# Performance work log

Hardware: AMD Instinct MI355X
Metric: run time of the kernel (lower is better)

## Reference

```python
import jax, jax.numpy as jnp
import numpy as np

N_NODES = 50000
N_EDGES = 800000
N_GRAPHS = 128
F_IN = 36
HEADS1 = 10
OUT_DIM = 128


def _gat_layer(x, src, dst, W, a_src, a_dst, b, heads, out_c):
    # x: [N, Fin]; W: [Fin, heads*out_c]; a_src/a_dst: [heads, out_c]; b: [heads*out_c]
    N = x.shape[0]
    h = (x @ W).reshape(N, heads, out_c)                      # [N,H,C]
    al_s = jnp.einsum('nhc,hc->nh', h, a_src)                 # [N,H]
    al_d = jnp.einsum('nhc,hc->nh', h, a_dst)                 # [N,H]
    e = jax.nn.leaky_relu(al_s[src] + al_d[dst], negative_slope=0.2)  # [E,H]
    # segment-softmax over incoming edges of each dst node
    m = jax.ops.segment_max(e, dst, num_segments=N)
    m = jnp.where(jnp.isfinite(m), m, 0.0)
    p = jnp.exp(e - m[dst])
    s = jax.ops.segment_sum(p, dst, num_segments=N)
    alpha = p / (s[dst] + 1e-16)                              # [E,H]
    out = jax.ops.segment_sum(alpha[:, :, None] * h[src], dst, num_segments=N)  # [N,H,C]
    return out.reshape(N, heads * out_c) + b


def setup_inputs() -> dict:
    key = jax.random.key(0)
    ks = jax.random.split(key, 12)
    x = jax.random.normal(ks[0], (N_NODES, F_IN), dtype=jnp.float32)
    edge_index = jax.random.randint(ks[1], (2, N_EDGES), 0, N_NODES, dtype=jnp.int64)
    batch = jnp.sort(jax.random.randint(ks[2], (N_NODES,), 0, N_GRAPHS, dtype=jnp.int64))
    g = 0.1  # glorot-ish scale
    W1 = jax.random.normal(ks[3], (F_IN, HEADS1 * F_IN), dtype=jnp.float32) * g
    att_src1 = jax.random.normal(ks[4], (HEADS1, F_IN), dtype=jnp.float32) * g
    att_dst1 = jax.random.normal(ks[5], (HEADS1, F_IN), dtype=jnp.float32) * g
    b1 = jnp.zeros((HEADS1 * F_IN,), dtype=jnp.float32)
    W2 = jax.random.normal(ks[6], (HEADS1 * F_IN, OUT_DIM), dtype=jnp.float32) * g
    att_src2 = jax.random.normal(ks[7], (1, OUT_DIM), dtype=jnp.float32) * g
    att_dst2 = jax.random.normal(ks[8], (1, OUT_DIM), dtype=jnp.float32) * g
    b2 = jnp.zeros((OUT_DIM,), dtype=jnp.float32)
    fc_w = jax.random.normal(ks[9], (OUT_DIM, OUT_DIM), dtype=jnp.float32) * g
    fc_b = jnp.zeros((OUT_DIM,), dtype=jnp.float32)
    return {"x": x, "edge_index": edge_index, "batch": batch,
            "W1": W1, "att_src1": att_src1, "att_dst1": att_dst1, "b1": b1,
            "W2": W2, "att_src2": att_src2, "att_dst2": att_dst2, "b2": b2,
            "fc_w": fc_w, "fc_b": fc_b}


def reference(x, edge_index, batch, W1, att_src1, att_dst1, b1,
              W2, att_src2, att_dst2, b2, fc_w, fc_b):
    N = x.shape[0]
    # PyG GATConv adds self loops by default
    loops = jnp.arange(N, dtype=edge_index.dtype)
    src = jnp.concatenate([edge_index[0], loops])
    dst = jnp.concatenate([edge_index[1], loops])
    # eval mode: dropouts are identity
    h = jax.nn.elu(_gat_layer(x, src, dst, W1, att_src1, att_dst1, b1, HEADS1, F_IN))
    h = _gat_layer(h, src, dst, W2, att_src2, att_dst2, b2, 1, OUT_DIM)
    h = jax.nn.relu(h)
    # global max pool over graphs
    g = jax.ops.segment_max(h, batch, num_segments=N_GRAPHS)
    g = jnp.where(jnp.isfinite(g), g, 0.0)
    out = jax.nn.relu(g @ fc_w + fc_b)
    return out
```

## Files before the change

kernel.cpp:

```cpp
#include <hip/hip_runtime.h>
#include <hip/hip_fp16.h>
#include <math.h>

#define N_NODES  50000
#define N_EDGES  800000
#define E_TOT    850000
#define N_GRAPHS 128
#define F_IN     36
#define NH1      10
#define C1       36
#define D1       360
#define D2       128

#define SCHUNK  512
#define NCHUNK  98

typedef unsigned int u32;

#if defined(__has_builtin)
#if __has_builtin(__builtin_amdgcn_fdot2)
#define HAVE_FDOT2 1
#endif
#endif
#ifndef HAVE_FDOT2
#define HAVE_FDOT2 0
#endif

typedef _Float16 h2v __attribute__((ext_vector_type(2)));

static __device__ __forceinline__ float2 h2f(u32 u) {
  __half2 h = __builtin_bit_cast(__half2, u);
  return __half22float2(h);
}
static __device__ __forceinline__ u32 f2h2(float a, float b) {
  __half2 h = __floats2half2_rn(a, b);
  return __builtin_bit_cast(u32, h);
}
static __device__ __forceinline__ float dot2acc(u32 a, u32 b, float acc) {
#if HAVE_FDOT2
  return __builtin_amdgcn_fdot2(__builtin_bit_cast(h2v, a), __builtin_bit_cast(h2v, b), acc, false);
#else
  float2 fa = h2f(a), fb = h2f(b);
  return fmaf(fa.x, fb.x, fmaf(fa.y, fb.y, acc));
#endif
}

__global__ void k_init(int* counts, u32* pool) {
  int i = blockIdx.x * blockDim.x + threadIdx.x;
  if (i < N_NODES) counts[i] = 0;
  if (i < N_GRAPHS * D2) pool[i] = 0u;
}

__global__ void k_hist(const int* ei, int* counts) {
  int e = blockIdx.x * blockDim.x + threadIdx.x;
  if (e >= E_TOT) return;
  int d = (e < N_EDGES) ? ei[N_EDGES + e] : (e - N_EDGES);
  atomicAdd(&counts[d], 1);
}

__global__ void k_scan1(const int* counts, int* partial) {
  __shared__ int red[256];
  int b = blockIdx.x, t = threadIdx.x;
  int base = b * SCHUNK;
  int v = 0;
  int i0 = base + t, i1 = base + t + 256;
  if (i0 < N_NODES) v += counts[i0];
  if (i1 < N_NODES) v += counts[i1];
  red[t] = v; __syncthreads();
  for (int off = 128; off; off >>= 1) {
    if (t < off) red[t] += red[t + off];
    __syncthreads();
  }
  if (t == 0) partial[b] = red[0];
}

__global__ void k_scan2(const int* partial, int* chunk_off, int* row_ptr) {
  if (threadIdx.x == 0 && blockIdx.x == 0) {
    int acc = 0;
    for (int i = 0; i < NCHUNK; i++) { chunk_off[i] = acc; acc += partial[i]; }
    row_ptr[N_NODES] = acc;
  }
}

__global__ void k_scan3(const int* counts, const int* chunk_off, int* row_ptr, int* nxt) {
  __shared__ int tmp[SCHUNK];
  int b = blockIdx.x, t = threadIdx.x;
  int i = b * SCHUNK + t;
  int v = (i < N_NODES) ? counts[i] : 0;
  tmp[t] = v; __syncthreads();
  for (int off = 1; off < SCHUNK; off <<= 1) {
    int x = (t >= off) ? tmp[t - off] : 0;
    __syncthreads();
    tmp[t] += x;
    __syncthreads();
  }
  if (i < N_NODES) {
    int excl = chunk_off[b] + tmp[t] - v;
    row_ptr[i] = excl;
    nxt[i] = excl;
  }
}

__global__ void k_scatter(const int* ei, int* nxt, int* csr_src) {
  int e = blockIdx.x * blockDim.x + threadIdx.x;
  if (e >= E_TOT) return;
  int s, d;
  if (e < N_EDGES) { s = ei[e]; d = ei[N_EDGES + e]; }
  else             { s = d = e - N_EDGES; }
  int pos = atomicAdd(&nxt[d], 1);
  csr_src[pos] = s;
}

__global__ void k_wals(const float* __restrict__ W1, const float* __restrict__ asrc,
                       const float* __restrict__ adst, float* w_als, float* w_ald) {
  int i = blockIdx.x * blockDim.x + threadIdx.x;
  if (i >= D1) return;
  int h = i / F_IN, k = i - h * F_IN;
  float sa = 0.f, sd = 0.f;
  for (int c = 0; c < C1; c++) {
    float wv = W1[k * D1 + h * C1 + c];
    sa = fmaf(wv, asrc[h * C1 + c], sa);
    sd = fmaf(wv, adst[h * C1 + c], sd);
  }
  w_als[i] = sa; w_ald[i] = sd;
}

__global__ void k_w1t2(const float* __restrict__ W1, u32* __restrict__ W1t2) {
  int i = blockIdx.x * blockDim.x + threadIdx.x;
  if (i >= D1 * (F_IN / 2)) return;
  int hc = i / (F_IN / 2), kp = i - hc * (F_IN / 2);
  W1t2[i] = f2h2(W1[(2 * kp) * D1 + hc], W1[(2 * kp + 1) * D1 + hc]);
}

__global__ void k_xh(const float* __restrict__ x, u32* __restrict__ xh2) {
  int i = blockIdx.x * blockDim.x + threadIdx.x;
  if (i >= N_NODES * F_IN / 2) return;
  xh2[i] = f2h2(x[2 * i], x[2 * i + 1]);
}

__global__ void k_packw2(const float* __restrict__ W2, u32* __restrict__ W2h) {
  int i = blockIdx.x * blockDim.x + threadIdx.x;
  if (i >= (D1 / 2) * D2) return;
  int kp = i / D2, col = i - kp * D2;
  W2h[i] = f2h2(W2[(2 * kp) * D2 + col], W2[(2 * kp + 1) * D2 + col]);
}

__global__ __launch_bounds__(256)
void k_als1(const float* __restrict__ x, const float* __restrict__ w_als,
            const float* __restrict__ w_ald, float* als, float* ald) {
  __shared__ float xs[64][F_IN + 1];
  __shared__ float wa[D1], wd[D1];
  int t = threadIdx.x;
  int nb = blockIdx.x * 64;
  for (int i = t; i < D1; i += 256) { wa[i] = w_als[i]; wd[i] = w_ald[i]; }
  int lim = min(64, N_NODES - nb);
  for (int i = t; i < lim * F_IN; i += 256) {
    int n = i / F_IN, k = i - n * F_IN;
    xs[n][k] = x[(size_t)(nb + n) * F_IN + k];
  }
  __syncthreads();
  for (int pair = t; pair < lim * NH1; pair += 256) {
    int n = pair / NH1, h = pair - n * NH1;
    const float* xp = xs[n];
    const float* wap = &wa[h * F_IN];
    const float* wdp = &wd[h * F_IN];
    float sa = 0.f, sd = 0.f;
#pragma unroll
    for (int k = 0; k < F_IN; k++) {
      float xv = xp[k];
      sa = fmaf(xv, wap[k], sa);
      sd = fmaf(xv, wdp[k], sd);
    }
    als[(size_t)(nb + n) * NH1 + h] = sa;
    ald[(size_t)(nb + n) * NH1 + h] = sd;
  }
}

__global__ __launch_bounds__(256)
void k_agg1(const __half* __restrict__ xh, const float* __restrict__ als,
            const float* __restrict__ ald, const int* __restrict__ row_ptr,
            const int* __restrict__ csr_src, __half* __restrict__ aggxh) {
  __shared__ float pl[4][64][NH1];
  __shared__ int ssrc[4][64];
  int w = threadIdx.x >> 6, lane = threadIdx.x & 63;
  int node = blockIdx.x * 4 + w;
  int beg = row_ptr[node], end = row_ptr[node + 1];

  int ch[6], hd[6];
#pragma unroll
  for (int j = 0; j < 6; j++) {
    int slot = lane + 64 * j;
    if (slot >= D1) slot = D1 - 1;
    hd[j] = slot / C1;
    ch[j] = slot - hd[j] * C1;
  }
  bool v5 = (lane < D1 - 320);

  float aldn[NH1];
#pragma unroll
  for (int h = 0; h < NH1; h++) aldn[h] = ald[(size_t)node * NH1 + h];
  float acc[6] = {0.f, 0.f, 0.f, 0.f, 0.f, 0.f};
  float sp[NH1];
#pragma unroll
  for (int h = 0; h < NH1; h++) sp[h] = 0.f;

  for (int base = beg; base < end; base += 64) {
    int cnt = min(64, end - base);
    float p[NH1];
    int msrc = 0;
    if (lane < cnt) {
      msrc = csr_src[base + lane];
      const float2* ap = (const float2*)(als + (size_t)msrc * NH1);
#pragma unroll
      for (int q = 0; q < 5; q++) {
        float2 v = ap[q];
        float v0 = v.x + aldn[2 * q];
        float v1 = v.y + aldn[2 * q + 1];
        v0 = v0 > 0.f ? v0 : 0.2f * v0;
        v1 = v1 > 0.f ? v1 : 0.2f * v1;
        p[2 * q] = __expf(v0);
        p[2 * q + 1] = __expf(v1);
      }
    } else {
#pragma unroll
      for (int h = 0; h < NH1; h++) p[h] = 0.f;
    }
#pragma unroll
    for (int h = 0; h < NH1; h++) sp[h] += p[h];
    ssrc[w][lane] = msrc;
    float2* plw = (float2*)pl[w][lane];
#pragma unroll
    for (int q = 0; q < 5; q++) plw[q] = float2{p[2 * q], p[2 * q + 1]};
    __builtin_amdgcn_wave_barrier();

    for (int j = 0; j < cnt; j++) {
      int srcj = ssrc[w][j];
      const __half* row = xh + (size_t)srcj * F_IN;
      const float* plj = pl[w][j];
#pragma unroll
      for (int jj = 0; jj < 6; jj++) {
        if (jj < 5 || v5) {
          float xv = __half2float(row[ch[jj]]);
          acc[jj] = fmaf(plj[hd[jj]], xv, acc[jj]);
        }
      }
    }
    __builtin_amdgcn_wave_barrier();
  }

#pragma unroll
  for (int h = 0; h < NH1; h++) {
    float t = sp[h];
#pragma unroll
    for (int off = 32; off; off >>= 1) t += __shfl_xor(t, off);
    sp[h] = t;
  }
#pragma unroll
  for (int jj = 0; jj < 6; jj++) {
    if (jj < 5 || v5) {
      float inv = 1.f / (sp[hd[jj]] + 1e-16f);
      aggxh[(size_t)node * D1 + lane + 64 * jj] = __float2half(acc[jj] * inv);
    }
  }
}

#define MIX_NPB 32
__global__ __launch_bounds__(384)
void k_mix1(const u32* __restrict__ aggx2, const u32* __restrict__ W1t2,
            const float* __restrict__ b1, __half* __restrict__ hact) {
  __shared__ u32 ag[MIX_NPB][D1 / 2 + 4];
  int t = threadIdx.x;
  int nb = blockIdx.x * MIX_NPB;
  int lim = min(MIX_NPB, N_NODES - nb);
  const u32* gsrc = aggx2 + (size_t)nb * (D1 / 2);
  for (int i = t; i < lim * (D1 / 2); i += 384) {
    int n = i / (D1 / 2), k = i - n * (D1 / 2);
    ag[n][k] = gsrc[i];
  }
  __syncthreads();
  if (t < D1) {
    int h = t / C1;
    u32 wreg[F_IN / 2];
#pragma unroll
    for (int kp = 0; kp < F_IN / 2; kp++) wreg[kp] = W1t2[t * (F_IN / 2) + kp];
    float bj = b1[t];
    for (int n = 0; n < lim; n++) {
      const u32* a = &ag[n][h * (F_IN / 2)];
      float acc2 = 0.f;
#pragma unroll
      for (int kp = 0; kp < F_IN / 2; kp++) acc2 = dot2acc(a[kp], wreg[kp], acc2);
      float val = acc2 + bj;
      val = val > 0.f ? val : __expf(val) - 1.f;
      hact[(size_t)(nb + n) * D1 + t] = __float2half(val);
    }
  }
}

#define G2_NPB 16
__global__ __launch_bounds__(256)
void k_gemm2(const __half* __restrict__ hacth, const u32* __restrict__ W2h,
             __half* __restrict__ h2h) {
  __shared__ u32 hs2[D1 / 2][G2_NPB];
  int nb = blockIdx.x * G2_NPB;
  int t = threadIdx.x;
  for (int i = t; i < G2_NPB * (D1 / 2); i += 256) {
    int n = i / (D1 / 2), kp = i - n * (D1 / 2);
    hs2[kp][n] = ((const u32*)(hacth + (size_t)(nb + n) * D1))[kp];
  }
  __syncthreads();
  int col = t & 127, ng = t >> 7;
  float acc[8];
#pragma unroll
  for (int i = 0; i < 8; i++) acc[i] = 0.f;
#pragma unroll 2
  for (int kp = 0; kp < D1 / 2; kp++) {
    u32 wv = W2h[kp * D2 + col];
    uint4 r0 = *(const uint4*)&hs2[kp][ng * 8];
    uint4 r1 = *(const uint4*)&hs2[kp][ng * 8 + 4];
    acc[0] = dot2acc(r0.x, wv, acc[0]);
    acc[1] = dot2acc(r0.y, wv, acc[1]);
    acc[2] = dot2acc(r0.z, wv, acc[2]);
    acc[3] = dot2acc(r0.w, wv, acc[3]);
    acc[4] = dot2acc(r1.x, wv, acc[4]);
    acc[5] = dot2acc(r1.y, wv, acc[5]);
    acc[6] = dot2acc(r1.z, wv, acc[6]);
    acc[7] = dot2acc(r1.w, wv, acc[7]);
  }
#pragma unroll
  for (int i = 0; i < 8; i++)
    h2h[(size_t)(nb + ng * 8 + i) * D2 + col] = __float2half(acc[i]);
}

__global__ void k_als2(const __half* __restrict__ h2h, const float* __restrict__ asrc,
                       const float* __restrict__ adst, float* als, float* ald) {
  int node = blockIdx.x * 4 + (threadIdx.x >> 6);
  int lane = threadIdx.x & 63;
  const u32* hr = (const u32*)(h2h + (size_t)node * D2);
  float2 f = h2f(hr[lane]);
  float2 a = ((const float2*)asrc)[lane];
  float2 d = ((const float2*)adst)[lane];
  float ps = f.x * a.x + f.y * a.y;
  float pd = f.x * d.x + f.y * d.y;
#pragma unroll
  for (int off = 32; off; off >>= 1) { ps += __shfl_xor(ps, off); pd += __shfl_xor(pd, off); }
  if (lane == 0) { als[node] = ps; ald[node] = pd; }
}

__global__ __launch_bounds__(256)
void k_agg2(const __half* __restrict__ h2h, const float* __restrict__ als,
            const float* __restrict__ ald, const int* __restrict__ row_ptr,
            const int* __restrict__ csr_src, const float* __restrict__ b2,
            const int* __restrict__ batch, u32* __restrict__ pool) {
  int w = threadIdx.x >> 6, lane = threadIdx.x & 63;
  int node = blockIdx.x * 4 + w;
  int beg = row_ptr[node], end = row_ptr[node + 1];
  float aldn = ald[node];
  float ax = 0.f, ay = 0.f, ssum = 0.f;
  for (int base = beg; base < end; base += 64) {
    int cnt = min(64, end - base);
    int msrc = 0; float p = 0.f;
    if (lane < cnt) {
      msrc = csr_src[base + lane];
      float vv = als[msrc] + aldn;
      vv = vv > 0.f ? vv : 0.2f * vv;
      p = __expf(vv);
    }
    ssum += p;
    int j2 = 0;
    for (; j2 + 2 <= cnt; j2 += 2) {
      int sA = __shfl(msrc, j2), sB = __shfl(msrc, j2 + 1);
      float cA = __shfl(p, j2), cB = __shfl(p, j2 + 1);
      u32 ua = ((const u32*)(h2h + (size_t)sA * D2))[lane];
      u32 ub = ((const u32*)(h2h + (size_t)sB * D2))[lane];
      float2 f = h2f(ua); ax = fmaf(cA, f.x, ax); ay = fmaf(cA, f.y, ay);
      f = h2f(ub); ax = fmaf(cB, f.x, ax); ay = fmaf(cB, f.y, ay);
    }
    if (j2 < cnt) {
      int sA = __shfl(msrc, j2);
      float cA = __shfl(p, j2);
      u32 ua = ((const u32*)(h2h + (size_t)sA * D2))[lane];
      float2 f = h2f(ua); ax = fmaf(cA, f.x, ax); ay = fmaf(cA, f.y, ay);
    }
  }
  float t2 = ssum;
#pragma unroll
  for (int off = 32; off; off >>= 1) t2 += __shfl_xor(t2, off);
  float inv = 1.f / (t2 + 1e-16f);
  float2 bv = ((const float2*)b2)[lane];
  float vx = fmaxf(ax * inv + bv.x, 0.f);
  float vy = fmaxf(ay * inv + bv.y, 0.f);
  int g = batch[node];
  atomicMax(&pool[g * D2 + 2 * lane], __float_as_uint(vx));
  atomicMax(&pool[g * D2 + 2 * lane + 1], __float_as_uint(vy));
}

__global__ void k_final(const float* __restrict__ pool, const float* __restrict__ fcw,
                        const float* __restrict__ fcb, float* __restrict__ out) {
  __shared__ float ps[D2];
  int g = blockIdx.x, j = threadIdx.x;
  ps[j] = pool[g * D2 + j];
  __syncthreads();
  float acc = 0.f;
  for (int c = 0; c < D2; c++) acc = fmaf(ps[c], fcw[c * D2 + j], acc);
  acc += fcb[j];
  out[g * D2 + j] = acc > 0.f ? acc : 0.f;
}

extern "C" void kernel_launch(void* const* d_in, const int* in_sizes, int n_in,
                              void* d_out, int out_size, void* d_ws, size_t ws_size,
                              hipStream_t stream) {
  const float* x     = (const float*)d_in[0];
  const int*   ei    = (const int*)d_in[1];
  const int*   batch = (const int*)d_in[2];
  const float* W1    = (const float*)d_in[3];
  const float* asrc1 = (const float*)d_in[4];
  const float* adst1 = (const float*)d_in[5];
  const float* b1    = (const float*)d_in[6];
  const float* W2    = (const float*)d_in[7];
  const float* asrc2 = (const float*)d_in[8];
  const float* adst2 = (const float*)d_in[9];
  const float* b2    = (const float*)d_in[10];
  const float* fcw   = (const float*)d_in[11];
  const float* fcb   = (const float*)d_in[12];
  float* out = (float*)d_out;

  char* w = (char*)d_ws;
  size_t off = 0;
  auto alloc = [&](size_t bytes) -> char* {
    char* p = w + off;
    off = (off + bytes + 255) & ~(size_t)255;
    return p;
  };
  int* counts    = (int*)alloc((size_t)N_NODES * 4);
  int* row_ptr   = (int*)alloc((size_t)(N_NODES + 1) * 4);
  int* nxt       = (int*)alloc((size_t)N_NODES * 4);
  int* csr_src   = (int*)alloc((size_t)E_TOT * 4);
  int* partial   = (int*)alloc(NCHUNK * 4);
  int* chunk_off = (int*)alloc(NCHUNK * 4);
  float* als1    = (float*)alloc((size_t)N_NODES * NH1 * 4);
  float* ald1    = (float*)alloc((size_t)N_NODES * NH1 * 4);
  float* als2    = (float*)alloc((size_t)N_NODES * 4);
  float* ald2    = (float*)alloc((size_t)N_NODES * 4);
  u32*   pool    = (u32*)alloc((size_t)N_GRAPHS * D2 * 4);
  float* w_als   = (float*)alloc((size_t)D1 * 4);
  float* w_ald   = (float*)alloc((size_t)D1 * 4);
  u32*   W1t2    = (u32*)alloc((size_t)D1 * (F_IN / 2) * 4);
  u32*   W2h     = (u32*)alloc((size_t)(D1 / 2) * D2 * 4);
  u32*   xh2     = (u32*)alloc((size_t)N_NODES * (F_IN / 2) * 4);
  u32*   aggx2   = (u32*)alloc((size_t)N_NODES * (D1 / 2) * 4);
  __half* hacth  = (__half*)alloc((size_t)N_NODES * D1 * 2);
  __half* h2h    = (__half*)alloc((size_t)N_NODES * D2 * 2);

  k_init<<<dim3(196), dim3(256), 0, stream>>>(counts, pool);
  k_hist<<<dim3((E_TOT + 255) / 256), dim3(256), 0, stream>>>(ei, counts);
  k_scan1<<<dim3(NCHUNK), dim3(256), 0, stream>>>(counts, partial);
  k_scan2<<<dim3(1), dim3(64), 0, stream>>>(partial, chunk_off, row_ptr);
  k_scan3<<<dim3(NCHUNK), dim3(SCHUNK), 0, stream>>>(counts, chunk_off, row_ptr, nxt);
  k_scatter<<<dim3((E_TOT + 255) / 256), dim3(256), 0, stream>>>(ei, nxt, csr_src);

  k_wals<<<dim3(2), dim3(256), 0, stream>>>(W1, asrc1, adst1, w_als, w_ald);
  k_w1t2<<<dim3((D1 * (F_IN / 2) + 255) / 256), dim3(256), 0, stream>>>(W1, W1t2);
  k_packw2<<<dim3(((D1 / 2) * D2 + 255) / 256), dim3(256), 0, stream>>>(W2, W2h);
  k_xh<<<dim3((N_NODES * F_IN / 2 + 255) / 256), dim3(256), 0, stream>>>(x, xh2);

  k_als1<<<dim3((N_NODES + 63) / 64), dim3(256), 0, stream>>>(x, w_als, w_ald, als1, ald1);
  k_agg1<<<dim3(N_NODES / 4), dim3(256), 0, stream>>>((const __half*)xh2, als1, ald1,
                                                      row_ptr, csr_src, (__half*)aggx2);
  k_mix1<<<dim3((N_NODES + MIX_NPB - 1) / MIX_NPB), dim3(384), 0, stream>>>(aggx2, W1t2, b1, hacth);

  k_gemm2<<<dim3(N_NODES / G2_NPB), dim3(256), 0, stream>>>(hacth, W2h, h2h);
  k_als2<<<dim3(N_NODES / 4), dim3(256), 0, stream>>>(h2h, asrc2, adst2, als2, ald2);
  k_agg2<<<dim3(N_NODES / 4), dim3(256), 0, stream>>>(h2h, als2, ald2, row_ptr, csr_src,
                                                      b2, batch, pool);

  k_final<<<dim3(N_GRAPHS), dim3(D2), 0, stream>>>((const float*)pool, fcw, fcb, out);

  (void)in_sizes; (void)n_in; (void)out_size; (void)ws_size;
}
```

Before: 552.0 us.

## Fuse weight prep kernels, fold x half-conversion into als1, vectorize agg1 gather

Merges the three weight-preparation kernels into one launch and moves the x-to-half conversion into k_als1, which already stages x in shared memory. This removes several launches and one extra pass over x. The layer-1 aggregation now has each lane handle half2 channel pairs (3 slots per lane instead of 6 scalar halves) and broadcasts source indices via shuffles instead of shared memory. It also unrolls the neighbor loop by two to raise memory-level parallelism, at the cost of more registers.

```diff
diff --git a/kernel.cpp b/kernel.cpp
--- a/kernel.cpp
+++ b/kernel.cpp
@@ -11,6 +11,7 @@
 #define C1       36
 #define D1       360
 #define D2       128
+#define XW       18
 
 #define SCHUNK  512
 #define NCHUNK  98
@@ -111,43 +112,34 @@
   csr_src[pos] = s;
 }
 
-__global__ void k_wals(const float* __restrict__ W1, const float* __restrict__ asrc,
-                       const float* __restrict__ adst, float* w_als, float* w_ald) {
-  int i = blockIdx.x * blockDim.x + threadIdx.x;
-  if (i >= D1) return;
-  int h = i / F_IN, k = i - h * F_IN;
-  float sa = 0.f, sd = 0.f;
-  for (int c = 0; c < C1; c++) {
-    float wv = W1[k * D1 + h * C1 + c];
-    sa = fmaf(wv, asrc[h * C1 + c], sa);
-    sd = fmaf(wv, adst[h * C1 + c], sd);
-  }
-  w_als[i] = sa; w_ald[i] = sd;
-}
-
-__global__ void k_w1t2(const float* __restrict__ W1, u32* __restrict__ W1t2) {
-  int i = blockIdx.x * blockDim.x + threadIdx.x;
-  if (i >= D1 * (F_IN / 2)) return;
-  int hc = i / (F_IN / 2), kp = i - hc * (F_IN / 2);
-  W1t2[i] = f2h2(W1[(2 * kp) * D1 + hc], W1[(2 * kp + 1) * D1 + hc]);
-}
-
-__global__ void k_xh(const float* __restrict__ x, u32* __restrict__ xh2) {
-  int i = blockIdx.x * blockDim.x + threadIdx.x;
-  if (i >= N_NODES * F_IN / 2) return;
-  xh2[i] = f2h2(x[2 * i], x[2 * i + 1]);
-}
-
-__global__ void k_packw2(const float* __restrict__ W2, u32* __restrict__ W2h) {
-  int i = blockIdx.x * blockDim.x + threadIdx.x;
-  if (i >= (D1 / 2) * D2) return;
-  int kp = i / D2, col = i - kp * D2;
-  W2h[i] = f2h2(W2[(2 * kp) * D2 + col], W2[(2 * kp + 1) * D2 + col]);
+__global__ void k_prep(const float* __restrict__ W1, const float* __restrict__ asrc,
+                       const float* __restrict__ adst, const float* __restrict__ W2,
+                       float* w_als, float* w_ald, u32* W1t2, u32* W2h) {
+  int id = blockIdx.x * blockDim.x + threadIdx.x;
+  if (id < D1) {
+    int h = id / F_IN, k = id - h * F_IN;
+    float sa = 0.f, sd = 0.f;
+    for (int c = 0; c < C1; c++) {
+      float wv = W1[k * D1 + h * C1 + c];
+      sa = fmaf(wv, asrc[h * C1 + c], sa);
+      sd = fmaf(wv, adst[h * C1 + c], sd);
+    }
+    w_als[id] = sa; w_ald[id] = sd;
+  } else if (id < D1 + D1 * (F_IN / 2)) {
+    int i = id - D1;
+    int hc = i / (F_IN / 2), kp = i - hc * (F_IN / 2);
+    W1t2[i] = f2h2(W1[(2 * kp) * D1 + hc], W1[(2 * kp + 1) * D1 + hc]);
+  } else if (id < D1 + D1 * (F_IN / 2) + (D1 / 2) * D2) {
+    int i = id - D1 - D1 * (F_IN / 2);
+    int kp = i / D2, col = i - kp * D2;
+    W2h[i] = f2h2(W2[(2 * kp) * D2 + col], W2[(2 * kp + 1) * D2 + col]);
+  }
 }
 
 __global__ __launch_bounds__(256)
 void k_als1(const float* __restrict__ x, const float* __restrict__ w_als,
-            const float* __restrict__ w_ald, float* als, float* ald) {
+            const float* __restrict__ w_ald, float* als, float* ald,
+            u32* __restrict__ xh2) {
   __shared__ float xs[64][F_IN + 1];
   __shared__ float wa[D1], wd[D1];
   int t = threadIdx.x;
@@ -159,6 +151,10 @@
     xs[n][k] = x[(size_t)(nb + n) * F_IN + k];
   }
   __syncthreads();
+  for (int i = t; i < lim * XW; i += 256) {
+    int n = i / XW, kp = i - n * XW;
+    xh2[(size_t)(nb + n) * XW + kp] = f2h2(xs[n][2 * kp], xs[n][2 * kp + 1]);
+  }
   for (int pair = t; pair < lim * NH1; pair += 256) {
     int n = pair / NH1, h = pair - n * NH1;
     const float* xp = xs[n];
@@ -177,29 +173,25 @@
 }
 
 __global__ __launch_bounds__(256)
-void k_agg1(const __half* __restrict__ xh, const float* __restrict__ als,
+void k_agg1(const u32* __restrict__ xrow, const float* __restrict__ als,
             const float* __restrict__ ald, const int* __restrict__ row_ptr,
-            const int* __restrict__ csr_src, __half* __restrict__ aggxh) {
+            const int* __restrict__ csr_src, u32* __restrict__ aggx2) {
   __shared__ float pl[4][64][NH1];
-  __shared__ int ssrc[4][64];
   int w = threadIdx.x >> 6, lane = threadIdx.x & 63;
   int node = blockIdx.x * 4 + w;
   int beg = row_ptr[node], end = row_ptr[node + 1];
 
-  int ch[6], hd[6];
-#pragma unroll
-  for (int j = 0; j < 6; j++) {
-    int slot = lane + 64 * j;
-    if (slot >= D1) slot = D1 - 1;
-    hd[j] = slot / C1;
-    ch[j] = slot - hd[j] * C1;
-  }
-  bool v5 = (lane < D1 - 320);
+  int h0 = lane / XW,  kp0 = lane - XW * h0;
+  int s1 = lane + 64;
+  int h1i = s1 / XW,   kp1 = s1 - XW * h1i;
+  bool v2 = lane < 52;
+  int s2 = v2 ? lane + 128 : 179;
+  int h2i = s2 / XW,   kp2 = s2 - XW * h2i;
 
   float aldn[NH1];
 #pragma unroll
   for (int h = 0; h < NH1; h++) aldn[h] = ald[(size_t)node * NH1 + h];
-  float acc[6] = {0.f, 0.f, 0.f, 0.f, 0.f, 0.f};
+  float a0x = 0.f, a0y = 0.f, a1x = 0.f, a1y = 0.f, a2x = 0.f, a2y = 0.f;
   float sp[NH1];
 #pragma unroll
   for (int h = 0; h < NH1; h++) sp[h] = 0.f;
@@ -227,23 +219,40 @@
     }
 #pragma unroll
     for (int h = 0; h < NH1; h++) sp[h] += p[h];
-    ssrc[w][lane] = msrc;
     float2* plw = (float2*)pl[w][lane];
 #pragma unroll
     for (int q = 0; q < 5; q++) plw[q] = float2{p[2 * q], p[2 * q + 1]};
     __builtin_amdgcn_wave_barrier();
 
-    for (int j = 0; j < cnt; j++) {
-      int srcj = ssrc[w][j];
-      const __half* row = xh + (size_t)srcj * F_IN;
-      const float* plj = pl[w][j];
-#pragma unroll
-      for (int jj = 0; jj < 6; jj++) {
-        if (jj < 5 || v5) {
-          float xv = __half2float(row[ch[jj]]);
-          acc[jj] = fmaf(plj[hd[jj]], xv, acc[jj]);
-        }
-      }
+    int j2 = 0;
+    for (; j2 + 2 <= cnt; j2 += 2) {
+      int sA = __shfl(msrc, j2), sB = __shfl(msrc, j2 + 1);
+      const u32* ra = xrow + (size_t)sA * XW;
+      const u32* rb = xrow + (size_t)sB * XW;
+      u32 ua0 = ra[kp0], ua1 = ra[kp1], ua2 = ra[kp2];
+      u32 ub0 = rb[kp0], ub1 = rb[kp1], ub2 = rb[kp2];
+      const float* pA = pl[w][j2];
+      const float* pB = pl[w][j2 + 1];
+      float cA0 = pA[h0], cA1 = pA[h1i], cA2 = pA[h2i];
+      float cB0 = pB[h0], cB1 = pB[h1i], cB2 = pB[h2i];
+      float2 f;
+      f = h2f(ua0); a0x = fmaf(cA0, f.x, a0x); a0y = fmaf(cA0, f.y, a0y);
+      f = h2f(ua1); a1x = fmaf(cA1, f.x, a1x); a1y = fmaf(cA1, f.y, a1y);
+      f = h2f(ua2); a2x = fmaf(cA2, f.x, a2x); a2y = fmaf(cA2, f.y, a2y);
+      f = h2f(ub0); a0x = fmaf(cB0, f.x, a0x); a0y = fmaf(cB0, f.y, a0y);
+      f = h2f(ub1); a1x = fmaf(cB1, f.x, a1x); a1y = fmaf(cB1, f.y, a1y);
+      f = h2f(ub2); a2x = fmaf(cB2, f.x, a2x); a2y = fmaf(cB2, f.y, a2y);
+    }
+    if (j2 < cnt) {
+      int sA = __shfl(msrc, j2);
+      const u32* ra = xrow + (size_t)sA * XW;
+      u32 ua0 = ra[kp0], ua1 = ra[kp1], ua2 = ra[kp2];
+      const float* pA = pl[w][j2];
+      float cA0 = pA[h0], cA1 = pA[h1i], cA2 = pA[h2i];
+      float2 f;
+      f = h2f(ua0); a0x = fmaf(cA0, f.x, a0x); a0y = fmaf(cA0, f.y, a0y);
+      f = h2f(ua1); a1x = fmaf(cA1, f.x, a1x); a1y = fmaf(cA1, f.y, a1y);
+      f = h2f(ua2); a2x = fmaf(cA2, f.x, a2x); a2y = fmaf(cA2, f.y, a2y);
     }
     __builtin_amdgcn_wave_barrier();
   }
@@ -255,13 +264,13 @@
     for (int off = 32; off; off >>= 1) t += __shfl_xor(t, off);
     sp[h] = t;
   }
-#pragma unroll
-  for (int jj = 0; jj < 6; jj++) {
-    if (jj < 5 || v5) {
-      float inv = 1.f / (sp[hd[jj]] + 1e-16f);
-      aggxh[(size_t)node * D1 + lane + 64 * jj] = __float2half(acc[jj] * inv);
-    }
-  }
+  float i0 = 1.f / (sp[h0] + 1e-16f);
+  float i1 = 1.f / (sp[h1i] + 1e-16f);
+  float i2 = 1.f / (sp[h2i] + 1e-16f);
+  u32* orow = aggx2 + (size_t)node * (D1 / 2);
+  orow[lane] = f2h2(a0x * i0, a0y * i0);
+  orow[lane + 64] = f2h2(a1x * i1, a1y * i1);
+  if (v2) orow[lane + 128] = f2h2(a2x * i2, a2y * i2);
 }
 
 #define MIX_NPB 32
@@ -446,7 +455,7 @@
   float* w_ald   = (float*)alloc((size_t)D1 * 4);
   u32*   W1t2    = (u32*)alloc((size_t)D1 * (F_IN / 2) * 4);
   u32*   W2h     = (u32*)alloc((size_t)(D1 / 2) * D2 * 4);
-  u32*   xh2     = (u32*)alloc((size_t)N_NODES * (F_IN / 2) * 4);
+  u32*   xh2     = (u32*)alloc((size_t)N_NODES * XW * 4);
   u32*   aggx2   = (u32*)alloc((size_t)N_NODES * (D1 / 2) * 4);
   __half* hacth  = (__half*)alloc((size_t)N_NODES * D1 * 2);
   __half* h2h    = (__half*)alloc((size_t)N_NODES * D2 * 2);
@@ -457,15 +466,10 @@
   k_scan2<<<dim3(1), dim3(64), 0, stream>>>(partial, chunk_off, row_ptr);
   k_scan3<<<dim3(NCHUNK), dim3(SCHUNK), 0, stream>>>(counts, chunk_off, row_ptr, nxt);
   k_scatter<<<dim3((E_TOT + 255) / 256), dim3(256), 0, stream>>>(ei, nxt, csr_src);
-
-  k_wals<<<dim3(2), dim3(256), 0, stream>>>(W1, asrc1, adst1, w_als, w_ald);
-  k_w1t2<<<dim3((D1 * (F_IN / 2) + 255) / 256), dim3(256), 0, stream>>>(W1, W1t2);
-  k_packw2<<<dim3(((D1 / 2) * D2 + 255) / 256), dim3(256), 0, stream>>>(W2, W2h);
-  k_xh<<<dim3((N_NODES * F_IN / 2 + 255) / 256), dim3(256), 0, stream>>>(x, xh2);
-
-  k_als1<<<dim3((N_NODES + 63) / 64), dim3(256), 0, stream>>>(x, w_als, w_ald, als1, ald1);
-  k_agg1<<<dim3(N_NODES / 4), dim3(256), 0, stream>>>((const __half*)xh2, als1, ald1,
-                                                      row_ptr, csr_src, (__half*)aggx2);
+  k_prep<<<dim3(117), dim3(256), 0, stream>>>(W1, asrc1, adst1, W2, w_als, w_ald, W1t2, W2h);
+
+  k_als1<<<dim3((N_NODES + 63) / 64), dim3(256), 0, stream>>>(x, w_als, w_ald, als1, ald1, xh2);
+  k_agg1<<<dim3(N_NODES / 4), dim3(256), 0, stream>>>(xh2, als1, ald1, row_ptr, csr_src, aggx2);
   k_mix1<<<dim3((N_NODES + MIX_NPB - 1) / MIX_NPB), dim3(384), 0, stream>>>(aggx2, W1t2, b1, hacth);
 
   k_gemm2<<<dim3(N_NODES / G2_NPB), dim3(256), 0, stream>>>(hacth, W2h, h2h);
```

After: 481.2 us. 1.15x faster.
